# Optimization experiments

Measured on AMD Instinct MI355X. Metric: run time of the kernel, lower is better.

## Reference

```python
import jax, jax.numpy as jnp
import numpy as np


def _d2(a, b):
    # squared euclidean distances, clamped at 0 (matches _full_cdist before sqrt)
    a2 = jnp.sum(a * a, axis=1)[:, None]
    b2 = jnp.sum(b * b, axis=1)[None, :]
    return jnp.clip(a2 + b2 - 2.0 * (a @ b.T), 0.0, None)


def _node_weights(pts, w1, b1, w2, b2):
    h = jax.nn.relu(pts @ w1 + b1)
    logits = h @ w2 + b2
    w = jax.nn.softplus(logits) + 1e-6
    w = w / jnp.sum(w)
    return w[:, 0]


def setup_inputs() -> dict:
    key = jax.random.key(0)
    ks = jax.random.split(key, 8)
    N, M, D, H, S = 8192, 8192, 2, 32, 3
    return {
        "base_points": jax.random.normal(ks[0], (N, D), jnp.float32),
        "target_points": jax.random.normal(ks[1], (M, D), jnp.float32),
        "log_sigmas": jnp.log(jnp.array([0.05, 0.1, 0.2], jnp.float32)),
        "log_scale": 0.1 * jax.random.normal(ks[2], (D,), jnp.float32),
        "wn_w1": jax.random.normal(ks[3], (D, H), jnp.float32) / np.sqrt(D),
        "wn_b1": jnp.zeros((H,), jnp.float32),
        "wn_w2": jax.random.normal(ks[4], (H, 1), jnp.float32) / np.sqrt(H),
        "wn_b2": jnp.zeros((1,), jnp.float32),
        "g_w1": jax.random.normal(ks[5], (4, H), jnp.float32) / 2.0,
        "g_b1": jnp.zeros((H,), jnp.float32),
        "g_w2": jax.random.normal(ks[6], (H, S), jnp.float32) / np.sqrt(H),
        "g_b2": jnp.zeros((S,), jnp.float32),
        "bias": jnp.zeros((1,), jnp.float32),
    }


def reference(base_points, target_points, log_sigmas, log_scale,
              wn_w1, wn_b1, wn_w2, wn_b2,
              g_w1, g_b1, g_w2, g_b2, bias):
    # learned anisotropic per-axis scale
    scale = jnp.exp(log_scale)
    base = base_points * scale
    target = target_points * scale

    # learned positive, normalized node weights (shared weight_net)
    w_b = _node_weights(base, wn_w1, wn_b1, wn_w2, wn_b2)
    w_t = _node_weights(target, wn_w1, wn_b1, wn_w2, wn_b2)

    # kde_mmd_loss with center=True: subtract weighted mean of each cloud.
    bc = base - jnp.sum(w_b[:, None] * base, axis=0)
    tc = target - jnp.sum(w_t[:, None] * target, axis=0)

    # squared distances computed ONCE, reused across all sigma bands
    d2_aa = _d2(bc, bc)
    d2_bb = _d2(tc, tc)
    d2_ab = _d2(bc, tc)

    sigmas = jnp.exp(log_sigmas)

    def band_loss(sigma):
        inv = 1.0 / (2.0 * sigma * sigma)
        kaa = jnp.exp(-d2_aa * inv)
        kbb = jnp.exp(-d2_bb * inv)
        kab = jnp.exp(-d2_ab * inv)
        # weighted MMD^2: w_a K_aa w_a + w_b K_bb w_b - 2 w_a K_ab w_b
        return (w_b @ (kaa @ w_b) + w_t @ (kbb @ w_t)
                - 2.0 * (w_b @ (kab @ w_t)))

    per_band = jnp.stack([band_loss(sigmas[i]) for i in range(sigmas.shape[0])])

    # gating statistics (torch.tensor([...]) detaches -> stop_gradient)
    dist = jnp.sqrt(_d2(base, target))
    mean_dist = jnp.mean(dist)
    var_dist = jnp.var(dist, ddof=1)  # torch .var() is unbiased
    n_base = base_points.shape[0]
    size_diff = abs(float(n_base - target_points.shape[0])) / (n_base + 1e-6)
    weight_var = jnp.var(w_b, ddof=1) + jnp.var(w_t, ddof=1)
    stats = jax.lax.stop_gradient(
        jnp.stack([mean_dist, var_dist,
                   jnp.asarray(size_diff, base.dtype), weight_var]))

    mix_logits = jax.nn.relu(stats @ g_w1 + g_b1) @ g_w2 + g_b2
    gw = jax.nn.softplus(mix_logits)
    gw = gw / jnp.sum(gw)
    return jnp.sum(gw * per_band) + bias[0]
```

## Files before the change

kernel.cpp:

```cpp
#include <hip/hip_runtime.h>
#include <math.h>

#define JT 64
#define ITILE 1024
#define T8 8
#define NJOB_AB 1024
#define NJOB_TRI 576
#define NBLK (NJOB_AB + 2 * NJOB_TRI)
#define L2E 1.4426950408889634f

typedef float v2f __attribute__((ext_vector_type(2)));

__device__ inline float fexp2n(float x) {
  float r;
  asm("v_exp_f32 %0, -%1" : "=v"(r) : "v"(x));
  return r;
}
__device__ inline float fsqrt(float x) {
  float r;
  asm("v_sqrt_f32 %0, %1" : "=v"(r) : "v"(x));
  return r;
}

__device__ inline double wred_d(double v) {
#pragma unroll
  for (int o = 32; o > 0; o >>= 1) v += __shfl_down(v, o, 64);
  return v;
}

__device__ inline double bred(double v, double* sm) {
  v = wred_d(v);
  __syncthreads();
  if ((threadIdx.x & 63) == 0) sm[threadIdx.x >> 6] = v;
  __syncthreads();
  return sm[0] + sm[1] + sm[2] + sm[3];
}

__device__ inline void slot_reduce(const double* slot, double* smean) {
  if (threadIdx.x < 64) {
    int l = threadIdx.x;
    const double* sl = slot + l * 4;
#pragma unroll
    for (int c = 0; c < 4; ++c) {
      double v = sl[c];
      double vb = (l < 32) ? v : 0.0;
      double vt = (l < 32) ? 0.0 : v;
      vb = wred_d(vb);
      vt = wred_d(vt);
      if (l == 0) {
        smean[c] = vb;
        smean[4 + c] = vt;
      }
    }
  }
}

__global__ __launch_bounds__(256) void prep_kernel(
    const float* __restrict__ base, const float* __restrict__ target,
    const float* __restrict__ log_sigmas, const float* __restrict__ log_scale,
    const float* __restrict__ w1, const float* __restrict__ b1,
    const float* __restrict__ w2, const float* __restrict__ b2,
    float2* __restrict__ pxy, float* __restrict__ pu,
    double* __restrict__ slot, unsigned* __restrict__ fctr, int n) {
  __shared__ double sm[4];
  int gid = blockIdx.x * 256 + threadIdx.x;
  int isT = gid >= n;
  const float* pts = isT ? target : base;
  int idx = isT ? gid - n : gid;
  float ex = __expf(log_scale[0]);
  float ey = __expf(log_scale[1]);
  float s2 = __expf(log_sigmas[2]);
  float r2 = __fsqrt_rn(L2E / (2.f * s2 * s2));
  float2 p = ((const float2*)pts)[idx];
  float xr = p.x * ex, yr = p.y * ey;
  float logit = b2[0];
#pragma unroll
  for (int k = 0; k < 32; ++k) {
    float h = fmaf(xr, w1[k], fmaf(yr, w1[32 + k], b1[k]));
    h = fmaxf(h, 0.f);
    logit = fmaf(h, w2[k], logit);
  }
  float u = fmaxf(logit, 0.f) + log1pf(__expf(-fabsf(logit))) + 1e-6f;
  float X = xr * r2, Y = yr * r2;
  pxy[gid] = make_float2(X, Y);
  pu[gid] = u;
  double su = bred((double)u, sm);
  double qu = bred((double)u * (double)u, sm);
  double mx = bred((double)u * (double)X, sm);
  double my = bred((double)u * (double)Y, sm);
  if (threadIdx.x == 0) {
    double* s = slot + blockIdx.x * 4;
    s[0] = su;
    s[1] = qu;
    s[2] = mx;
    s[3] = my;
    if (blockIdx.x == 0) *fctr = 0u;
  }
}

template <bool AB, bool FAST>
__device__ inline void tile_loop(const float* sx, const float* sy,
                                 const float* su, const float* snb,
                                 const v2f xi2[4], const v2f yi2[4],
                                 const v2f al2[4], float rr0, float rr1,
                                 v2f a0[4], v2f a1[4], v2f a2[4], float& sdo,
                                 float& sqo) {
  float sda = 0.f, sdb = 0.f;
  v2f sq2 = {0.f, 0.f};
  const v2f vz = {0.f, 0.f};
#pragma unroll 2
  for (int jj = 0; jj < JT / 2; ++jj) {
    v2f xj = *(const v2f*)&sx[2 * jj];
    v2f yj = *(const v2f*)&sy[2 * jj];
    v2f uj = *(const v2f*)&su[2 * jj];
    v2f nbj;
    if constexpr (AB) nbj = *(const v2f*)&snb[2 * jj];
#pragma unroll
    for (int i = 0; i < 4; ++i) {
      v2f dx = xi2[i] - xj;
      v2f dy = yi2[i] - yj;
      v2f pos = dx * dx + dy * dy;
      v2f k2 = {fexp2n(pos.x), fexp2n(pos.y)};
      v2f k0, k1;
      if constexpr (FAST) {
        v2f t = k2 * k2;
        k1 = t * t;
        v2f t1 = k1 * k1;
        k0 = t1 * t1;
      } else {
        v2f m1 = pos * rr1;
        v2f m0 = pos * rr0;
        k1 = {fexp2n(m1.x), fexp2n(m1.y)};
        k0 = {fexp2n(m0.x), fexp2n(m0.y)};
      }
      a0[i] += uj * k0;
      a1[i] += uj * k1;
      a2[i] += uj * k2;
      if constexpr (AB) {
        v2f anb = al2[i] + nbj;
        v2f d2u = pos + anb;
        d2u = __builtin_elementwise_max(d2u, vz);
        sq2 += d2u;
        sda += fsqrt(d2u.x);
        sdb += fsqrt(d2u.y);
      }
    }
  }
  sdo = sda + sdb;
  sqo = sq2.x + sq2.y;
}

__global__ __launch_bounds__(256) void pair_kernel(
    const float2* __restrict__ pxy, const float* __restrict__ pu,
    const double* __restrict__ slot, double* __restrict__ paa,
    double* __restrict__ pbb, double* __restrict__ pab,
    double* __restrict__ psd, double* __restrict__ psq,
    unsigned* __restrict__ fctr, const float* __restrict__ log_sigmas,
    const float* __restrict__ g_w1, const float* __restrict__ g_b1,
    const float* __restrict__ g_w2, const float* __restrict__ g_b2,
    const float* __restrict__ bias, float* __restrict__ out, int n) {
  __shared__ __align__(16) float sx[JT];
  __shared__ __align__(16) float sy[JT];
  __shared__ __align__(16) float su[JT];
  __shared__ __align__(16) float snb[JT];
  __shared__ double sm[4];
  __shared__ double smean[8];
  __shared__ int lastf;

  int b = blockIdx.x;
  int m, it, jt = 0, j0, pidx;
  if (b < NJOB_AB) {
    m = 2;
    pidx = b;
    it = b >> 7;
    j0 = (b & 127) * JT;
  } else {
    int r = b - NJOB_AB;
    m = (r < NJOB_TRI) ? 0 : 1;
    if (m == 1) r -= NJOB_TRI;
    pidx = r;
    int tile = r >> 4;
    int q = r & 15;
    int idx = tile, len = T8;
    it = 0;
    while (idx >= len) {
      idx -= len;
      --len;
      ++it;
    }
    jt = it + idx;
    j0 = jt * ITILE + q * JT;
  }
  const float2* pxyI = pxy + ((m == 1) ? n : 0);
  const float* puI = pu + ((m == 1) ? n : 0);
  const float2* pxyJ = pxy + ((m == 0) ? 0 : n);
  const float* puJ = pu + ((m == 0) ? 0 : n);

  float cx = 0.f, cy = 0.f, cx2 = 0.f, cy2 = 0.f, cc = 0.f;
  if (m == 2) {
    slot_reduce(slot, smean);
  }

  float s0 = __expf(log_sigmas[0]);
  float s1 = __expf(log_sigmas[1]);
  float s2 = __expf(log_sigmas[2]);
  float rr0 = (s2 * s2) / (s0 * s0);
  float rr1 = (s2 * s2) / (s1 * s1);
  bool fast = (fabsf(rr0 - 16.f) <= 0.016f) && (fabsf(rr1 - 4.f) <= 0.004f);

  if (m == 2) {
    __syncthreads();
    cx = (float)(smean[2] / smean[0] - smean[6] / smean[4]);
    cy = (float)(smean[3] / smean[0] - smean[7] / smean[4]);
    cx2 = 2.f * cx;
    cy2 = 2.f * cy;
    cc = cx * cx + cy * cy;
  }

  if (threadIdx.x < JT) {
    float2 v = pxyJ[j0 + threadIdx.x];
    sx[threadIdx.x] = v.x;
    sy[threadIdx.x] = v.y;
    su[threadIdx.x] = puJ[j0 + threadIdx.x];
    if (m == 2) snb[threadIdx.x] = -fmaf(cx2, v.x, cy2 * v.y);
  }
  __syncthreads();

  int i0 = it * ITILE + threadIdx.x;
  v2f xi2[4], yi2[4], al2[4];
  float u[4];
#pragma unroll
  for (int i = 0; i < 4; ++i) {
    float2 P = pxyI[i0 + i * 256];
    u[i] = puI[i0 + i * 256];
    float xv = P.x, yv = P.y, alv = 0.f;
    if (m == 2) {
      xv -= cx;
      yv -= cy;
      alv = fmaf(cx2, xv, cy2 * yv) + cc;
    }
    xi2[i] = (v2f){xv, xv};
    yi2[i] = (v2f){yv, yv};
    al2[i] = (v2f){alv, alv};
  }

  v2f a0[4] = {}, a1[4] = {}, a2[4] = {};
  float sd = 0.f, sq = 0.f;
  if (m == 2) {
    if (fast)
      tile_loop<true, true>(sx, sy, su, snb, xi2, yi2, al2, rr0, rr1, a0, a1,
                            a2, sd, sq);
    else
      tile_loop<true, false>(sx, sy, su, snb, xi2, yi2, al2, rr0, rr1, a0, a1,
                             a2, sd, sq);
  } else {
    if (fast)
      tile_loop<false, true>(sx, sy, su, snb, xi2, yi2, al2, rr0, rr1, a0, a1,
                             a2, sd, sq);
    else
      tile_loop<false, false>(sx, sy, su, snb, xi2, yi2, al2, rr0, rr1, a0,
                              a1, a2, sd, sq);
  }

  double wgt = (m != 2 && jt != it) ? 2.0 : 1.0;
  double c0 = 0.0, c1 = 0.0, c2 = 0.0;
#pragma unroll
  for (int i = 0; i < 4; ++i) {
    c0 += (double)u[i] * (double)(a0[i].x + a0[i].y);
    c1 += (double)u[i] * (double)(a1[i].x + a1[i].y);
    c2 += (double)u[i] * (double)(a2[i].x + a2[i].y);
  }
  double r0 = bred(c0, sm) * wgt;
  double r1 = bred(c1, sm) * wgt;
  double r2d = bred(c2, sm) * wgt;
  double* prow = (m == 0) ? paa : (m == 1) ? pbb : pab;
  int stride = (m == 2) ? NJOB_AB : NJOB_TRI;
  if (threadIdx.x == 0) {
    prow[0 * stride + pidx] = r0;
    prow[1 * stride + pidx] = r1;
    prow[2 * stride + pidx] = r2d;
  }
  if (m == 2) {
    double rsd = bred((double)sd, sm);
    double rsq = bred((double)sq, sm);
    if (threadIdx.x == 0) {
      psd[pidx] = rsd;
      psq[pidx] = rsq;
    }
  }

  if (threadIdx.x == 0) {
    __threadfence();
    unsigned old = atomicAdd(fctr, 1u);
    lastf = (old == NBLK - 1) ? 1 : 0;
  }
  __syncthreads();
  if (!lastf) return;
  __threadfence();

  slot_reduce(slot, smean);
  __syncthreads();
  int t = threadIdx.x;
  double vaa[3], vbb[3], vab[3];
  for (int s = 0; s < 3; ++s) {
    const double* pa = paa + s * NJOB_TRI;
    const double* pb = pbb + s * NJOB_TRI;
    const double* pc = pab + s * NJOB_AB;
    double va = pa[t] + pa[t + 256] + ((t < 64) ? pa[t + 512] : 0.0);
    double vb = pb[t] + pb[t + 256] + ((t < 64) ? pb[t + 512] : 0.0);
    double vc = pc[t] + pc[t + 256] + pc[t + 512] + pc[t + 768];
    vaa[s] = bred(va, sm);
    vbb[s] = bred(vb, sm);
    vab[s] = bred(vc, sm);
  }
  double sdt = bred(psd[t] + psd[t + 256] + psd[t + 512] + psd[t + 768], sm);
  double sqt = bred(psq[t] + psq[t + 256] + psq[t + 512] + psq[t + 768], sm);

  if (threadIdx.x == 0) {
    double Sb = smean[0], Qb = smean[1], St = smean[4], Qt = smean[5];
    double pband[3];
    for (int s = 0; s < 3; ++s)
      pband[s] = vaa[s] / (Sb * Sb) + vbb[s] / (St * St) -
                 2.0 * vab[s] / (Sb * St);
    double s2d = (double)s2;
    double r2sq = (double)L2E / (2.0 * s2d * s2d);
    double sd_real = sdt / sqrt(r2sq);
    double sq_real = sqt / r2sq;
    double NN = (double)n;
    double NM = NN * NN;
    double mean_d = sd_real / NM;
    double var_d = (sq_real - sd_real * sd_real / NM) / (NM - 1.0);
    double wv = (Qb / (Sb * Sb) - 1.0 / NN) / (NN - 1.0) +
                (Qt / (St * St) - 1.0 / NN) / (NN - 1.0);
    float st[4] = {(float)mean_d, (float)var_d, 0.f, (float)wv};
    float gl[3] = {g_b2[0], g_b2[1], g_b2[2]};
    for (int k = 0; k < 32; ++k) {
      float h = g_b1[k];
      for (int c = 0; c < 4; ++c) h = fmaf(st[c], g_w1[c * 32 + k], h);
      h = fmaxf(h, 0.f);
      for (int s = 0; s < 3; ++s) gl[s] = fmaf(h, g_w2[k * 3 + s], gl[s]);
    }
    float gw[3];
    float gsum = 0.f;
    for (int s = 0; s < 3; ++s) {
      gw[s] = fmaxf(gl[s], 0.f) + log1pf(__expf(-fabsf(gl[s])));
      gsum += gw[s];
    }
    double r = 0.0;
    for (int s = 0; s < 3; ++s) r += (double)(gw[s] / gsum) * pband[s];
    out[0] = (float)(r + (double)bias[0]);
  }
}

extern "C" void kernel_launch(void* const* d_in, const int* in_sizes, int n_in,
                              void* d_out, int out_size, void* d_ws,
                              size_t ws_size, hipStream_t stream) {
  const float* base = (const float*)d_in[0];
  const float* target = (const float*)d_in[1];
  const float* log_sigmas = (const float*)d_in[2];
  const float* log_scale = (const float*)d_in[3];
  const float* wn_w1 = (const float*)d_in[4];
  const float* wn_b1 = (const float*)d_in[5];
  const float* wn_w2 = (const float*)d_in[6];
  const float* wn_b2 = (const float*)d_in[7];
  const float* g_w1 = (const float*)d_in[8];
  const float* g_b1 = (const float*)d_in[9];
  const float* g_w2 = (const float*)d_in[10];
  const float* g_b2 = (const float*)d_in[11];
  const float* bias = (const float*)d_in[12];
  int n = in_sizes[0] / 2;

  double* dbase = (double*)d_ws;
  double* slot = dbase;
  double* paa = dbase + 256;
  double* pbb = paa + 3 * NJOB_TRI;
  double* pab = pbb + 3 * NJOB_TRI;
  double* psd = pab + 3 * NJOB_AB;
  double* psq = psd + NJOB_AB;
  double* dend = psq + NJOB_AB;
  float2* pxy = (float2*)dend;
  float* pu = (float*)(pxy + 2 * n);
  unsigned* fctr = (unsigned*)(pu + 2 * n);

  prep_kernel<<<(2 * n) / 256, 256, 0, stream>>>(
      base, target, log_sigmas, log_scale, wn_w1, wn_b1, wn_w2, wn_b2, pxy, pu,
      slot, fctr, n);
  pair_kernel<<<NBLK, 256, 0, stream>>>(pxy, pu, slot, paa, pbb, pab, psd, psq,
                                        fctr, log_sigmas, g_w1, g_b1, g_w2,
                                        g_b2, bias, (float*)d_out, n);
}
```

Measured before the change: 147.6 us.

## Use norm-expansion distances and 8 rows per thread with 128-thread blocks

Rewrites the pairwise squared distance as |xi|^2 + |xj|^2 - 2 xi·xj, precomputing per-row and per-column norms and doubled coordinates so the inner loop needs fewer VALU ops per pair. Each thread now holds 8 i-rows instead of 4, with blocks shrunk to 128 threads, which amortises the shared-memory loads of each j point over more rows. The final reductions are adjusted for the smaller block. The trade-off is more registers per thread, which may reduce occupancy, and the expanded form can lose precision for nearby points.

```diff
diff --git a/kernel.cpp b/kernel.cpp
--- a/kernel.cpp
+++ b/kernel.cpp
@@ -7,6 +7,7 @@
 #define NJOB_AB 1024
 #define NJOB_TRI 576
 #define NBLK (NJOB_AB + 2 * NJOB_TRI)
+#define NT 128
 #define L2E 1.4426950408889634f
 
 typedef float v2f __attribute__((ext_vector_type(2)));
@@ -28,12 +29,20 @@
   return v;
 }
 
-__device__ inline double bred(double v, double* sm) {
+__device__ inline double bred256(double v, double* sm) {
   v = wred_d(v);
   __syncthreads();
   if ((threadIdx.x & 63) == 0) sm[threadIdx.x >> 6] = v;
   __syncthreads();
   return sm[0] + sm[1] + sm[2] + sm[3];
+}
+
+__device__ inline double bred128(double v, double* sm) {
+  v = wred_d(v);
+  __syncthreads();
+  if ((threadIdx.x & 63) == 0) sm[threadIdx.x >> 6] = v;
+  __syncthreads();
+  return sm[0] + sm[1];
 }
 
 __device__ inline void slot_reduce(const double* slot, double* smean) {
@@ -84,10 +93,10 @@
   float X = xr * r2, Y = yr * r2;
   pxy[gid] = make_float2(X, Y);
   pu[gid] = u;
-  double su = bred((double)u, sm);
-  double qu = bred((double)u * (double)u, sm);
-  double mx = bred((double)u * (double)X, sm);
-  double my = bred((double)u * (double)Y, sm);
+  double su = bred256((double)u, sm);
+  double qu = bred256((double)u * (double)u, sm);
+  double mx = bred256((double)u * (double)X, sm);
+  double my = bred256((double)u * (double)Y, sm);
   if (threadIdx.x == 0) {
     double* s = slot + blockIdx.x * 4;
     s[0] = su;
@@ -100,12 +109,13 @@
 
 template <bool AB, bool FAST>
 __device__ inline void tile_loop(const float* sx, const float* sy,
-                                 const float* su, const float* snb,
-                                 const v2f xi2[4], const v2f yi2[4],
-                                 const v2f al2[4], float rr0, float rr1,
-                                 v2f a0[4], v2f a1[4], v2f a2[4], float& sdo,
+                                 const float* su, const float* sB,
+                                 const float* snb, const float xi2[8],
+                                 const float yi2[8], const float Ai[8],
+                                 const float al[8], float rr0, float rr1,
+                                 v2f a0[8], v2f a1[8], v2f a2[8], float& sdo,
                                  float& sqo) {
-  float sda = 0.f, sdb = 0.f;
+  v2f sd2 = {0.f, 0.f};
   v2f sq2 = {0.f, 0.f};
   const v2f vz = {0.f, 0.f};
 #pragma unroll 2
@@ -113,13 +123,15 @@
     v2f xj = *(const v2f*)&sx[2 * jj];
     v2f yj = *(const v2f*)&sy[2 * jj];
     v2f uj = *(const v2f*)&su[2 * jj];
+    v2f Bj = *(const v2f*)&sB[2 * jj];
     v2f nbj;
     if constexpr (AB) nbj = *(const v2f*)&snb[2 * jj];
 #pragma unroll
-    for (int i = 0; i < 4; ++i) {
-      v2f dx = xi2[i] - xj;
-      v2f dy = yi2[i] - yj;
-      v2f pos = dx * dx + dy * dy;
+    for (int i = 0; i < 8; ++i) {
+      v2f c = Bj + Ai[i];
+      v2f xi = {xi2[i], xi2[i]};
+      v2f yi = {yi2[i], yi2[i]};
+      v2f pos = c - xi * xj - yi * yj;
       v2f k2 = {fexp2n(pos.x), fexp2n(pos.y)};
       v2f k0, k1;
       if constexpr (FAST) {
@@ -137,20 +149,20 @@
       a1[i] += uj * k1;
       a2[i] += uj * k2;
       if constexpr (AB) {
-        v2f anb = al2[i] + nbj;
-        v2f d2u = pos + anb;
+        v2f ali = {al[i], al[i]};
+        v2f d2u = (pos + ali) + nbj;
         d2u = __builtin_elementwise_max(d2u, vz);
         sq2 += d2u;
-        sda += fsqrt(d2u.x);
-        sdb += fsqrt(d2u.y);
+        v2f rt = {fsqrt(d2u.x), fsqrt(d2u.y)};
+        sd2 += rt;
       }
     }
   }
-  sdo = sda + sdb;
+  sdo = sd2.x + sd2.y;
   sqo = sq2.x + sq2.y;
 }
 
-__global__ __launch_bounds__(256) void pair_kernel(
+__global__ __launch_bounds__(NT) void pair_kernel(
     const float2* __restrict__ pxy, const float* __restrict__ pu,
     const double* __restrict__ slot, double* __restrict__ paa,
     double* __restrict__ pbb, double* __restrict__ pab,
@@ -162,12 +174,14 @@
   __shared__ __align__(16) float sx[JT];
   __shared__ __align__(16) float sy[JT];
   __shared__ __align__(16) float su[JT];
+  __shared__ __align__(16) float sB[JT];
   __shared__ __align__(16) float snb[JT];
-  __shared__ double sm[4];
+  __shared__ double sm[2];
   __shared__ double smean[8];
   __shared__ int lastf;
 
   int b = blockIdx.x;
+  int tid = threadIdx.x;
   int m, it, jt = 0, j0, pidx;
   if (b < NJOB_AB) {
     m = 2;
@@ -217,79 +231,80 @@
     cc = cx * cx + cy * cy;
   }
 
-  if (threadIdx.x < JT) {
-    float2 v = pxyJ[j0 + threadIdx.x];
-    sx[threadIdx.x] = v.x;
-    sy[threadIdx.x] = v.y;
-    su[threadIdx.x] = puJ[j0 + threadIdx.x];
-    if (m == 2) snb[threadIdx.x] = -fmaf(cx2, v.x, cy2 * v.y);
-  }
-  __syncthreads();
-
-  int i0 = it * ITILE + threadIdx.x;
-  v2f xi2[4], yi2[4], al2[4];
-  float u[4];
-#pragma unroll
-  for (int i = 0; i < 4; ++i) {
-    float2 P = pxyI[i0 + i * 256];
-    u[i] = puI[i0 + i * 256];
-    float xv = P.x, yv = P.y, alv = 0.f;
+  if (tid < JT) {
+    float2 v = pxyJ[j0 + tid];
+    sx[tid] = v.x;
+    sy[tid] = v.y;
+    su[tid] = puJ[j0 + tid];
+    sB[tid] = fmaf(v.x, v.x, v.y * v.y);
+    if (m == 2) snb[tid] = -fmaf(cx2, v.x, cy2 * v.y);
+  }
+  __syncthreads();
+
+  int i0 = it * ITILE + tid;
+  float xi2[8], yi2[8], Ai[8], al[8];
+#pragma unroll
+  for (int i = 0; i < 8; ++i) {
+    float2 P = pxyI[i0 + i * NT];
+    float xv = P.x, yv = P.y;
+    al[i] = 0.f;
     if (m == 2) {
       xv -= cx;
       yv -= cy;
-      alv = fmaf(cx2, xv, cy2 * yv) + cc;
-    }
-    xi2[i] = (v2f){xv, xv};
-    yi2[i] = (v2f){yv, yv};
-    al2[i] = (v2f){alv, alv};
-  }
-
-  v2f a0[4] = {}, a1[4] = {}, a2[4] = {};
+      al[i] = fmaf(cx2, xv, cy2 * yv) + cc;
+    }
+    Ai[i] = fmaf(xv, xv, yv * yv);
+    xi2[i] = 2.f * xv;
+    yi2[i] = 2.f * yv;
+  }
+
+  v2f a0[8] = {}, a1[8] = {}, a2[8] = {};
   float sd = 0.f, sq = 0.f;
   if (m == 2) {
     if (fast)
-      tile_loop<true, true>(sx, sy, su, snb, xi2, yi2, al2, rr0, rr1, a0, a1,
-                            a2, sd, sq);
+      tile_loop<true, true>(sx, sy, su, sB, snb, xi2, yi2, Ai, al, rr0, rr1,
+                            a0, a1, a2, sd, sq);
     else
-      tile_loop<true, false>(sx, sy, su, snb, xi2, yi2, al2, rr0, rr1, a0, a1,
-                             a2, sd, sq);
+      tile_loop<true, false>(sx, sy, su, sB, snb, xi2, yi2, Ai, al, rr0, rr1,
+                             a0, a1, a2, sd, sq);
   } else {
     if (fast)
-      tile_loop<false, true>(sx, sy, su, snb, xi2, yi2, al2, rr0, rr1, a0, a1,
-                             a2, sd, sq);
+      tile_loop<false, true>(sx, sy, su, sB, snb, xi2, yi2, Ai, al, rr0, rr1,
+                             a0, a1, a2, sd, sq);
     else
-      tile_loop<false, false>(sx, sy, su, snb, xi2, yi2, al2, rr0, rr1, a0,
-                              a1, a2, sd, sq);
+      tile_loop<false, false>(sx, sy, su, sB, snb, xi2, yi2, Ai, al, rr0, rr1,
+                              a0, a1, a2, sd, sq);
   }
 
   double wgt = (m != 2 && jt != it) ? 2.0 : 1.0;
   double c0 = 0.0, c1 = 0.0, c2 = 0.0;
 #pragma unroll
-  for (int i = 0; i < 4; ++i) {
-    c0 += (double)u[i] * (double)(a0[i].x + a0[i].y);
-    c1 += (double)u[i] * (double)(a1[i].x + a1[i].y);
-    c2 += (double)u[i] * (double)(a2[i].x + a2[i].y);
-  }
-  double r0 = bred(c0, sm) * wgt;
-  double r1 = bred(c1, sm) * wgt;
-  double r2d = bred(c2, sm) * wgt;
+  for (int i = 0; i < 8; ++i) {
+    double ui = (double)puI[i0 + i * NT];
+    c0 += ui * (double)(a0[i].x + a0[i].y);
+    c1 += ui * (double)(a1[i].x + a1[i].y);
+    c2 += ui * (double)(a2[i].x + a2[i].y);
+  }
+  double r0 = bred128(c0, sm) * wgt;
+  double r1 = bred128(c1, sm) * wgt;
+  double r2d = bred128(c2, sm) * wgt;
   double* prow = (m == 0) ? paa : (m == 1) ? pbb : pab;
   int stride = (m == 2) ? NJOB_AB : NJOB_TRI;
-  if (threadIdx.x == 0) {
+  if (tid == 0) {
     prow[0 * stride + pidx] = r0;
     prow[1 * stride + pidx] = r1;
     prow[2 * stride + pidx] = r2d;
   }
   if (m == 2) {
-    double rsd = bred((double)sd, sm);
-    double rsq = bred((double)sq, sm);
-    if (threadIdx.x == 0) {
+    double rsd = bred128((double)sd, sm);
+    double rsq = bred128((double)sq, sm);
+    if (tid == 0) {
       psd[pidx] = rsd;
       psq[pidx] = rsq;
     }
   }
 
-  if (threadIdx.x == 0) {
+  if (tid == 0) {
     __threadfence();
     unsigned old = atomicAdd(fctr, 1u);
     lastf = (old == NBLK - 1) ? 1 : 0;
@@ -300,23 +315,33 @@
 
   slot_reduce(slot, smean);
   __syncthreads();
-  int t = threadIdx.x;
+  int t = tid;
   double vaa[3], vbb[3], vab[3];
   for (int s = 0; s < 3; ++s) {
     const double* pa = paa + s * NJOB_TRI;
     const double* pb = pbb + s * NJOB_TRI;
     const double* pc = pab + s * NJOB_AB;
-    double va = pa[t] + pa[t + 256] + ((t < 64) ? pa[t + 512] : 0.0);
-    double vb = pb[t] + pb[t + 256] + ((t < 64) ? pb[t + 512] : 0.0);
-    double vc = pc[t] + pc[t + 256] + pc[t + 512] + pc[t + 768];
-    vaa[s] = bred(va, sm);
-    vbb[s] = bred(vb, sm);
-    vab[s] = bred(vc, sm);
-  }
-  double sdt = bred(psd[t] + psd[t + 256] + psd[t + 512] + psd[t + 768], sm);
-  double sqt = bred(psq[t] + psq[t + 256] + psq[t + 512] + psq[t + 768], sm);
-
-  if (threadIdx.x == 0) {
+    double va = pa[t] + pa[t + 128] + pa[t + 256] + pa[t + 384] +
+                ((t < 64) ? pa[t + 512] : 0.0);
+    double vb = pb[t] + pb[t + 128] + pb[t + 256] + pb[t + 384] +
+                ((t < 64) ? pb[t + 512] : 0.0);
+    double vc = 0.0;
+#pragma unroll
+    for (int k = 0; k < 8; ++k) vc += pc[t + 128 * k];
+    vaa[s] = bred128(va, sm);
+    vbb[s] = bred128(vb, sm);
+    vab[s] = bred128(vc, sm);
+  }
+  double sdp = 0.0, sqp = 0.0;
+#pragma unroll
+  for (int k = 0; k < 8; ++k) {
+    sdp += psd[t + 128 * k];
+    sqp += psq[t + 128 * k];
+  }
+  double sdt = bred128(sdp, sm);
+  double sqt = bred128(sqp, sm);
+
+  if (tid == 0) {
     double Sb = smean[0], Qb = smean[1], St = smean[4], Qt = smean[5];
     double pband[3];
     for (int s = 0; s < 3; ++s)
@@ -385,7 +410,7 @@
   prep_kernel<<<(2 * n) / 256, 256, 0, stream>>>(
       base, target, log_sigmas, log_scale, wn_w1, wn_b1, wn_w2, wn_b2, pxy, pu,
       slot, fctr, n);
-  pair_kernel<<<NBLK, 256, 0, stream>>>(pxy, pu, slot, paa, pbb, pab, psd, psq,
-                                        fctr, log_sigmas, g_w1, g_b1, g_w2,
-                                        g_b2, bias, (float*)d_out, n);
-}
+  pair_kernel<<<NBLK, NT, 0, stream>>>(pxy, pu, slot, paa, pbb, pab, psd, psq,
+                                       fctr, log_sigmas, g_w1, g_b1, g_w2,
+                                       g_b2, bias, (float*)d_out, n);
+}
```

Result: slower. 167.7 us (+13.7%).

## Pack point data as float4 and expand squared distance algebraically

Applied to the files above, without the earlier changes.

The prep kernel now writes x, y, squared norm and weight as one float4 per point. The pair kernel reads j-points directly from global memory (uniform loads) instead of staging them in LDS behind a barrier. Distances are computed as |a|^2+|b|^2-2a·b, with the i-side factor of 2 and norms precomputed, cutting per-pair ops from sub/mul/fma to two FMAs. The i-values are packed so the accumulators pair two i-points per v2f rather than two j-points. The expanded form risks cancellation error for nearby points, and the per-j nb term is now recomputed in the inner loop.

```diff
diff --git a/kernel.cpp b/kernel.cpp
--- a/kernel.cpp
+++ b/kernel.cpp
@@ -60,8 +60,8 @@
     const float* __restrict__ log_sigmas, const float* __restrict__ log_scale,
     const float* __restrict__ w1, const float* __restrict__ b1,
     const float* __restrict__ w2, const float* __restrict__ b2,
-    float2* __restrict__ pxy, float* __restrict__ pu,
-    double* __restrict__ slot, unsigned* __restrict__ fctr, int n) {
+    float4* __restrict__ pxyu, double* __restrict__ slot,
+    unsigned* __restrict__ fctr, int n) {
   __shared__ double sm[4];
   int gid = blockIdx.x * 256 + threadIdx.x;
   int isT = gid >= n;
@@ -82,8 +82,8 @@
   }
   float u = fmaxf(logit, 0.f) + log1pf(__expf(-fabsf(logit))) + 1e-6f;
   float X = xr * r2, Y = yr * r2;
-  pxy[gid] = make_float2(X, Y);
-  pu[gid] = u;
+  float q = fmaf(X, X, Y * Y);
+  pxyu[gid] = make_float4(X, Y, q, u);
   double su = bred((double)u, sm);
   double qu = bred((double)u * (double)u, sm);
   double mx = bred((double)u * (double)X, sm);
@@ -99,27 +99,25 @@
 }
 
 template <bool AB, bool FAST>
-__device__ inline void tile_loop(const float* sx, const float* sy,
-                                 const float* su, const float* snb,
-                                 const v2f xi2[4], const v2f yi2[4],
-                                 const v2f al2[4], float rr0, float rr1,
-                                 v2f a0[4], v2f a1[4], v2f a2[4], float& sdo,
+__device__ inline void tile_loop(const float4* __restrict__ pJ4,
+                                 const v2f xi2[2], const v2f yi2[2],
+                                 const v2f Ai[2], const v2f al2[2], float cx2,
+                                 float cy2, float rr0, float rr1, v2f a0[2],
+                                 v2f a1[2], v2f a2[2], float& sdo,
                                  float& sqo) {
-  float sda = 0.f, sdb = 0.f;
+  v2f sd2 = {0.f, 0.f};
   v2f sq2 = {0.f, 0.f};
   const v2f vz = {0.f, 0.f};
-#pragma unroll 2
-  for (int jj = 0; jj < JT / 2; ++jj) {
-    v2f xj = *(const v2f*)&sx[2 * jj];
-    v2f yj = *(const v2f*)&sy[2 * jj];
-    v2f uj = *(const v2f*)&su[2 * jj];
-    v2f nbj;
-    if constexpr (AB) nbj = *(const v2f*)&snb[2 * jj];
-#pragma unroll
-    for (int i = 0; i < 4; ++i) {
-      v2f dx = xi2[i] - xj;
-      v2f dy = yi2[i] - yj;
-      v2f pos = dx * dx + dy * dy;
+#pragma unroll 4
+  for (int j = 0; j < JT; ++j) {
+    float4 J = pJ4[j];
+    float xj = J.x, yj = J.y, qj = J.z, uj = J.w;
+    float nbj;
+    if constexpr (AB) nbj = -fmaf(cx2, xj, cy2 * yj);
+#pragma unroll
+    for (int g = 0; g < 2; ++g) {
+      v2f c = Ai[g] + qj;
+      v2f pos = c - xi2[g] * xj - yi2[g] * yj;
       v2f k2 = {fexp2n(pos.x), fexp2n(pos.y)};
       v2f k0, k1;
       if constexpr (FAST) {
@@ -133,41 +131,37 @@
         k1 = {fexp2n(m1.x), fexp2n(m1.y)};
         k0 = {fexp2n(m0.x), fexp2n(m0.y)};
       }
-      a0[i] += uj * k0;
-      a1[i] += uj * k1;
-      a2[i] += uj * k2;
+      a0[g] += uj * k0;
+      a1[g] += uj * k1;
+      a2[g] += uj * k2;
       if constexpr (AB) {
-        v2f anb = al2[i] + nbj;
-        v2f d2u = pos + anb;
+        v2f d2u = (pos + al2[g]) + nbj;
         d2u = __builtin_elementwise_max(d2u, vz);
         sq2 += d2u;
-        sda += fsqrt(d2u.x);
-        sdb += fsqrt(d2u.y);
+        v2f rt = {fsqrt(d2u.x), fsqrt(d2u.y)};
+        sd2 += rt;
       }
     }
   }
-  sdo = sda + sdb;
+  sdo = sd2.x + sd2.y;
   sqo = sq2.x + sq2.y;
 }
 
 __global__ __launch_bounds__(256) void pair_kernel(
-    const float2* __restrict__ pxy, const float* __restrict__ pu,
-    const double* __restrict__ slot, double* __restrict__ paa,
-    double* __restrict__ pbb, double* __restrict__ pab,
-    double* __restrict__ psd, double* __restrict__ psq,
-    unsigned* __restrict__ fctr, const float* __restrict__ log_sigmas,
-    const float* __restrict__ g_w1, const float* __restrict__ g_b1,
-    const float* __restrict__ g_w2, const float* __restrict__ g_b2,
-    const float* __restrict__ bias, float* __restrict__ out, int n) {
-  __shared__ __align__(16) float sx[JT];
-  __shared__ __align__(16) float sy[JT];
-  __shared__ __align__(16) float su[JT];
-  __shared__ __align__(16) float snb[JT];
+    const float4* __restrict__ pxyu, const double* __restrict__ slot,
+    double* __restrict__ paa, double* __restrict__ pbb,
+    double* __restrict__ pab, double* __restrict__ psd,
+    double* __restrict__ psq, unsigned* __restrict__ fctr,
+    const float* __restrict__ log_sigmas, const float* __restrict__ g_w1,
+    const float* __restrict__ g_b1, const float* __restrict__ g_w2,
+    const float* __restrict__ g_b2, const float* __restrict__ bias,
+    float* __restrict__ out, int n) {
   __shared__ double sm[4];
   __shared__ double smean[8];
   __shared__ int lastf;
 
   int b = blockIdx.x;
+  int tid = threadIdx.x;
   int m, it, jt = 0, j0, pidx;
   if (b < NJOB_AB) {
     m = 2;
@@ -191,10 +185,8 @@
     jt = it + idx;
     j0 = jt * ITILE + q * JT;
   }
-  const float2* pxyI = pxy + ((m == 1) ? n : 0);
-  const float* puI = pu + ((m == 1) ? n : 0);
-  const float2* pxyJ = pxy + ((m == 0) ? 0 : n);
-  const float* puJ = pu + ((m == 0) ? 0 : n);
+  const float4* pI = pxyu + ((m == 1) ? n : 0);
+  const float4* pJ = pxyu + ((m == 0) ? 0 : n);
 
   float cx = 0.f, cy = 0.f, cx2 = 0.f, cy2 = 0.f, cc = 0.f;
   if (m == 2) {
@@ -217,48 +209,46 @@
     cc = cx * cx + cy * cy;
   }
 
-  if (threadIdx.x < JT) {
-    float2 v = pxyJ[j0 + threadIdx.x];
-    sx[threadIdx.x] = v.x;
-    sy[threadIdx.x] = v.y;
-    su[threadIdx.x] = puJ[j0 + threadIdx.x];
-    if (m == 2) snb[threadIdx.x] = -fmaf(cx2, v.x, cy2 * v.y);
-  }
-  __syncthreads();
-
-  int i0 = it * ITILE + threadIdx.x;
-  v2f xi2[4], yi2[4], al2[4];
+  int i0 = it * ITILE + tid;
+  v2f xi2[2], yi2[2], Ai[2], al2[2];
   float u[4];
 #pragma unroll
   for (int i = 0; i < 4; ++i) {
-    float2 P = pxyI[i0 + i * 256];
-    u[i] = puI[i0 + i * 256];
+    float4 P = pI[i0 + i * 256];
+    u[i] = P.w;
     float xv = P.x, yv = P.y, alv = 0.f;
+    float Av;
     if (m == 2) {
       xv -= cx;
       yv -= cy;
       alv = fmaf(cx2, xv, cy2 * yv) + cc;
-    }
-    xi2[i] = (v2f){xv, xv};
-    yi2[i] = (v2f){yv, yv};
-    al2[i] = (v2f){alv, alv};
-  }
-
-  v2f a0[4] = {}, a1[4] = {}, a2[4] = {};
+      Av = fmaf(xv, xv, yv * yv);
+    } else {
+      Av = P.z;
+    }
+    int g = i >> 1, h = i & 1;
+    xi2[g][h] = 2.f * xv;
+    yi2[g][h] = 2.f * yv;
+    Ai[g][h] = Av;
+    al2[g][h] = alv;
+  }
+
+  v2f a0[2] = {}, a1[2] = {}, a2[2] = {};
   float sd = 0.f, sq = 0.f;
+  const float4* pJ4 = pJ + j0;
   if (m == 2) {
     if (fast)
-      tile_loop<true, true>(sx, sy, su, snb, xi2, yi2, al2, rr0, rr1, a0, a1,
-                            a2, sd, sq);
+      tile_loop<true, true>(pJ4, xi2, yi2, Ai, al2, cx2, cy2, rr0, rr1, a0,
+                            a1, a2, sd, sq);
     else
-      tile_loop<true, false>(sx, sy, su, snb, xi2, yi2, al2, rr0, rr1, a0, a1,
-                             a2, sd, sq);
+      tile_loop<true, false>(pJ4, xi2, yi2, Ai, al2, cx2, cy2, rr0, rr1, a0,
+                             a1, a2, sd, sq);
   } else {
     if (fast)
-      tile_loop<false, true>(sx, sy, su, snb, xi2, yi2, al2, rr0, rr1, a0, a1,
-                             a2, sd, sq);
+      tile_loop<false, true>(pJ4, xi2, yi2, Ai, al2, cx2, cy2, rr0, rr1, a0,
+                             a1, a2, sd, sq);
     else
-      tile_loop<false, false>(sx, sy, su, snb, xi2, yi2, al2, rr0, rr1, a0,
+      tile_loop<false, false>(pJ4, xi2, yi2, Ai, al2, cx2, cy2, rr0, rr1, a0,
                               a1, a2, sd, sq);
   }
 
@@ -266,16 +256,17 @@
   double c0 = 0.0, c1 = 0.0, c2 = 0.0;
 #pragma unroll
   for (int i = 0; i < 4; ++i) {
-    c0 += (double)u[i] * (double)(a0[i].x + a0[i].y);
-    c1 += (double)u[i] * (double)(a1[i].x + a1[i].y);
-    c2 += (double)u[i] * (double)(a2[i].x + a2[i].y);
+    int g = i >> 1, h = i & 1;
+    c0 += (double)u[i] * (double)a0[g][h];
+    c1 += (double)u[i] * (double)a1[g][h];
+    c2 += (double)u[i] * (double)a2[g][h];
   }
   double r0 = bred(c0, sm) * wgt;
   double r1 = bred(c1, sm) * wgt;
   double r2d = bred(c2, sm) * wgt;
   double* prow = (m == 0) ? paa : (m == 1) ? pbb : pab;
   int stride = (m == 2) ? NJOB_AB : NJOB_TRI;
-  if (threadIdx.x == 0) {
+  if (tid == 0) {
     prow[0 * stride + pidx] = r0;
     prow[1 * stride + pidx] = r1;
     prow[2 * stride + pidx] = r2d;
@@ -283,13 +274,13 @@
   if (m == 2) {
     double rsd = bred((double)sd, sm);
     double rsq = bred((double)sq, sm);
-    if (threadIdx.x == 0) {
+    if (tid == 0) {
       psd[pidx] = rsd;
       psq[pidx] = rsq;
     }
   }
 
-  if (threadIdx.x == 0) {
+  if (tid == 0) {
     __threadfence();
     unsigned old = atomicAdd(fctr, 1u);
     lastf = (old == NBLK - 1) ? 1 : 0;
@@ -300,7 +291,7 @@
 
   slot_reduce(slot, smean);
   __syncthreads();
-  int t = threadIdx.x;
+  int t = tid;
   double vaa[3], vbb[3], vab[3];
   for (int s = 0; s < 3; ++s) {
     const double* pa = paa + s * NJOB_TRI;
@@ -316,7 +307,7 @@
   double sdt = bred(psd[t] + psd[t + 256] + psd[t + 512] + psd[t + 768], sm);
   double sqt = bred(psq[t] + psq[t + 256] + psq[t + 512] + psq[t + 768], sm);
 
-  if (threadIdx.x == 0) {
+  if (tid == 0) {
     double Sb = smean[0], Qb = smean[1], St = smean[4], Qt = smean[5];
     double pband[3];
     for (int s = 0; s < 3; ++s)
@@ -378,14 +369,13 @@
   double* psd = pab + 3 * NJOB_AB;
   double* psq = psd + NJOB_AB;
   double* dend = psq + NJOB_AB;
-  float2* pxy = (float2*)dend;
-  float* pu = (float*)(pxy + 2 * n);
-  unsigned* fctr = (unsigned*)(pu + 2 * n);
+  float4* pxyu = (float4*)dend;
+  unsigned* fctr = (unsigned*)(pxyu + 2 * n);
 
   prep_kernel<<<(2 * n) / 256, 256, 0, stream>>>(
-      base, target, log_sigmas, log_scale, wn_w1, wn_b1, wn_w2, wn_b2, pxy, pu,
+      base, target, log_sigmas, log_scale, wn_w1, wn_b1, wn_w2, wn_b2, pxyu,
       slot, fctr, n);
-  pair_kernel<<<NBLK, 256, 0, stream>>>(pxy, pu, slot, paa, pbb, pab, psd, psq,
+  pair_kernel<<<NBLK, 256, 0, stream>>>(pxyu, slot, paa, pbb, pab, psd, psq,
                                         fctr, log_sigmas, g_w1, g_b1, g_w2,
                                         g_b2, bias, (float*)d_out, n);
 }
```

Result: slower. 154.8 us (+4.9%).
